# Optimization experiments

Measured on AMD Instinct MI355X. Metric: run time of the kernel, lower is better.

Reference implementation:

```python
import jax, jax.numpy as jnp
import numpy as np

B, F, U, G = 2048, 512, 512, 64
REG_STRENGTH = 1.0


def setup_inputs() -> dict:
    key = jax.random.key(0)
    k0, k1, k2, k3, k4 = jax.random.split(key, 5)
    x = jax.random.normal(k0, (B, F), dtype=jnp.float32)
    gid = jax.random.randint(k1, (B,), 0, G, dtype=jnp.int64)
    # glorot-normal-ish scale for kernels: sqrt(2/(fan_in+fan_out))
    glorot = np.sqrt(2.0 / (U + F)).astype(np.float32)
    w_mu = jax.random.normal(k2, (G, U, F), dtype=jnp.float32) * glorot
    b_mu = jax.random.normal(k3, (G, U), dtype=jnp.float32) * 0.05  # 'random_normal' init
    w0_mu = jax.random.normal(k4, (U, F), dtype=jnp.float32) * glorot
    b0_mu = jnp.zeros((U,), dtype=jnp.float32)
    return {"x": x, "gid": gid, "w_mu": w_mu, "b_mu": b_mu, "w0_mu": w0_mu, "b0_mu": b0_mu}


def reference(x, gid, w_mu, b_mu, w0_mu, b0_mu):
    # Hard top-1 routing: per-sample weight matrix gather, [B, U, F]
    w = jnp.take(w_mu, gid, axis=0)
    b = jnp.take(b_mu, gid, axis=0)  # [B, U]
    # Batched matvec: 'Bup,Bp->Bu'
    outputs = jnp.einsum("buf,bf->bu", w, x) + b  # use_bias=True, activation=None
    # L2 prior regularization loss (added via add_loss in the original)
    w_loss = jnp.sum(jnp.square(w - w0_mu[None]))  # sum over axes [1,2] then batch
    b_loss = jnp.sum(jnp.square(b - b0_mu[None]))
    reg_loss = REG_STRENGTH * (w_loss + b_loss)
    return outputs, reg_loss
```

## Files before the change

kernel.cpp:

```cpp
#include <hip/hip_runtime.h>
#include <hip/hip_bf16.h>

#define B_SZ 2048
#define F_SZ 512
#define U_SZ 512
#define G_SZ 64
#define REG_STRENGTH 1.0f

#define BM 32
#define BN 64
#define BK 32
#define ZSPLIT 2
#define NTILES (U_SZ / BN)
#define THREADS 128


__global__ __launch_bounds__(1024) void prep_kernel(
    const int* __restrict__ gid, float* __restrict__ wsf,
    int* __restrict__ counts, int* __restrict__ rowstart,
    int* __restrict__ order) {
  __shared__ int cnt_s[G_SZ];
  __shared__ int cur_s[G_SZ];
  const int tid = threadIdx.x;

  if (tid < G_SZ) cnt_s[tid] = 0;
  if (tid == 0) wsf[0] = 0.0f;
  __syncthreads();

  for (int b = tid; b < B_SZ; b += 1024) atomicAdd(&cnt_s[gid[b]], 1);
  __syncthreads();

  if (tid == 0) {
    int run = 0;
    for (int g = 0; g < G_SZ; ++g) { cur_s[g] = run; run += cnt_s[g]; }
  }
  __syncthreads();

  if (tid < G_SZ) { counts[tid] = cnt_s[tid]; rowstart[tid] = cur_s[tid]; }
  __syncthreads();

  for (int b = tid; b < B_SZ; b += 1024) {
    int pos = atomicAdd(&cur_s[gid[b]], 1);
    order[pos] = b;
  }
}

__global__ __launch_bounds__(THREADS) void gemm_kernel(
    const float* __restrict__ x, const float* __restrict__ w_mu,
    const float* __restrict__ b_mu, const float* __restrict__ w0_mu,
    const float* __restrict__ b0_mu, float* __restrict__ out,
    float* __restrict__ wsf, const int* __restrict__ counts,
    const int* __restrict__ rowstart, const int* __restrict__ order) {
  const int g = blockIdx.y;
  const int cnt = counts[g];
  if (cnt == 0) return;
  const int z = blockIdx.z;
  const int n0 = blockIdx.x * BN;
  const int rs = rowstart[g];
  const int tid = threadIdx.x;

  const int tn = tid & 15;
  const int tmc = tid >> 4;
  const int sr = tid >> 3;
  const int skq = tid & 7;
  const int kb = skq * 4;

  __shared__ __align__(16) float Xs[BK][BM + 4];
  __shared__ __align__(16) float Ws[BK][BN + 4];

  const float* __restrict__ Wg = w_mu + (size_t)g * (U_SZ * F_SZ);
  const bool do_reg = (z == 0);
  float regp = 0.0f;

  if (do_reg && blockIdx.x == 0) {
    const float4 bm4 = *(const float4*)(b_mu + (g << 9) + tid * 4);
    const float4 b04 = *(const float4*)(b0_mu + tid * 4);
    float dx = bm4.x - b04.x, dy = bm4.y - b04.y;
    float dz = bm4.z - b04.z, dw = bm4.w - b04.w;
    regp += dx * dx + dy * dy + dz * dz + dw * dw;
  }

  bool first_pass = true;
  for (int r0 = z * BM; r0 < cnt; r0 += BM * ZSPLIT) {
    float acc[4][4] = {};
    int rA = r0 + sr;      if (rA >= cnt) rA = cnt - 1;
    int rB = r0 + sr + 16; if (rB >= cnt) rB = cnt - 1;
    const float* __restrict__ xrowA = x + (size_t)order[rs + rA] * F_SZ;
    const float* __restrict__ xrowB = x + (size_t)order[rs + rB] * F_SZ;

    float4 xpA = *(const float4*)(xrowA + kb);
    float4 xpB = *(const float4*)(xrowB + kb);
    float4 wp[4];
#pragma unroll
    for (int m = 0; m < 4; ++m)
      wp[m] = *(const float4*)(Wg + (size_t)(n0 + sr + 16 * m) * F_SZ + kb);

    for (int kc = 0; kc < F_SZ; kc += BK) {
      __syncthreads();
      Xs[kb + 0][sr] = xpA.x; Xs[kb + 1][sr] = xpA.y;
      Xs[kb + 2][sr] = xpA.z; Xs[kb + 3][sr] = xpA.w;
      Xs[kb + 0][sr + 16] = xpB.x; Xs[kb + 1][sr + 16] = xpB.y;
      Xs[kb + 2][sr + 16] = xpB.z; Xs[kb + 3][sr + 16] = xpB.w;
#pragma unroll
      for (int m = 0; m < 4; ++m) {
        const int u = sr + 16 * m;
        Ws[kb + 0][u] = wp[m].x; Ws[kb + 1][u] = wp[m].y;
        Ws[kb + 2][u] = wp[m].z; Ws[kb + 3][u] = wp[m].w;
      }
      if (do_reg && first_pass) {
#pragma unroll
        for (int m = 0; m < 4; ++m) {
          const float4 w04 = *(const float4*)(
              w0_mu + (size_t)(n0 + sr + 16 * m) * F_SZ + kc + kb);
          float dx = wp[m].x - w04.x, dy = wp[m].y - w04.y;
          float dz = wp[m].z - w04.z, dw = wp[m].w - w04.w;
          regp += dx * dx + dy * dy + dz * dz + dw * dw;
        }
      }
      __syncthreads();
      if (kc + BK < F_SZ) {
        const int ko = kc + BK + kb;
        xpA = *(const float4*)(xrowA + ko);
        xpB = *(const float4*)(xrowB + ko);
#pragma unroll
        for (int m = 0; m < 4; ++m)
          wp[m] = *(const float4*)(Wg + (size_t)(n0 + sr + 16 * m) * F_SZ + ko);
      }
#pragma unroll
      for (int kk = 0; kk < BK; ++kk) {
        const float4 av = *(const float4*)&Xs[kk][tmc * 4];
        const float4 bv = *(const float4*)&Ws[kk][tn * 4];
        const float a[4] = {av.x, av.y, av.z, av.w};
        const float b[4] = {bv.x, bv.y, bv.z, bv.w};
#pragma unroll
        for (int i = 0; i < 4; ++i)
#pragma unroll
          for (int j = 0; j < 4; ++j) acc[i][j] += a[i] * b[j];
      }
    }

    const float4 bias = *(const float4*)(b_mu + (g << 9) + n0 + tn * 4);
#pragma unroll
    for (int i = 0; i < 4; ++i) {
      const int r = r0 + tmc * 4 + i;
      if (r < cnt) {
        float4 o;
        o.x = acc[i][0] + bias.x;
        o.y = acc[i][1] + bias.y;
        o.z = acc[i][2] + bias.z;
        o.w = acc[i][3] + bias.w;
        *(float4*)(out + (size_t)order[rs + r] * U_SZ + n0 + tn * 4) = o;
      }
    }
    first_pass = false;
  }

  if (do_reg) {
    __syncthreads();
    float* red = &Xs[0][0];
    red[tid] = regp;
    __syncthreads();
    for (int s = 64; s > 0; s >>= 1) {
      if (tid < s) red[tid] += red[tid + s];
      __syncthreads();
    }
    if (tid == 0) atomicAdd(wsf, (float)cnt * red[0]);
  }
}

__global__ void finalize_kernel(const float* __restrict__ wsf,
                                float* __restrict__ out) {
  out[(size_t)B_SZ * U_SZ] = REG_STRENGTH * wsf[0];
}

extern "C" void kernel_launch(void* const* d_in, const int* in_sizes, int n_in,
                              void* d_out, int out_size, void* d_ws, size_t ws_size,
                              hipStream_t stream) {
  const float* x     = (const float*)d_in[0];
  const int*   gid   = (const int*)d_in[1];
  const float* w_mu  = (const float*)d_in[2];
  const float* b_mu  = (const float*)d_in[3];
  const float* w0_mu = (const float*)d_in[4];
  const float* b0_mu = (const float*)d_in[5];
  float* out = (float*)d_out;

  float* wsf      = (float*)d_ws;
  int*   counts   = (int*)d_ws + 2;
  int*   rowstart = (int*)d_ws + 2 + G_SZ;
  int*   order    = (int*)d_ws + 2 + 2 * G_SZ;

  prep_kernel<<<1, 1024, 0, stream>>>(gid, wsf, counts, rowstart, order);
  gemm_kernel<<<dim3(NTILES, G_SZ, ZSPLIT), THREADS, 0, stream>>>(
      x, w_mu, b_mu, w0_mu, b0_mu, out, wsf, counts, rowstart, order);
  finalize_kernel<<<1, 1, 0, stream>>>(wsf, out);
}
```

Before: 142.0 us.

## Use bf16 MFMA with chunk-scheduled grid and fused last-block finalize

Replaces the fp32 FMA tiled GEMM with bf16 MFMA 16x16x32 instructions. Inputs are converted to bf16 when staged into shared memory. The grid is rebuilt from a per-group chunk list of 64 rows, built in prep, instead of a fixed group-by-zsplit grid. The finalize kernel is dropped in favour of a last-block ticket, which saves one launch and cuts idle blocks. The cost is bf16 precision loss in the outputs, which may break tolerance, plus extra register use.

After: 174.8 us. 1.23x slower.

```diff
diff --git a/kernel.cpp b/kernel.cpp
--- a/kernel.cpp
+++ b/kernel.cpp
@@ -7,170 +7,210 @@
 #define G_SZ 64
 #define REG_STRENGTH 1.0f
 
-#define BM 32
+#define BM 64
 #define BN 64
-#define BK 32
-#define ZSPLIT 2
+#define BK 64
 #define NTILES (U_SZ / BN)
-#define THREADS 128
-
+#define MAXCHUNKS (B_SZ / BM + G_SZ)
+#define XSTR 72
+#define WSTR 72
+
+typedef __attribute__((ext_vector_type(8))) short bf16x8;
+typedef __attribute__((ext_vector_type(4))) float f32x4;
+
+#define WS_WSF      0
+#define WS_TICKET   1
+#define WS_NCH      2
+#define WS_COUNTS   4
+#define WS_ROWSTART (4 + G_SZ)
+#define WS_ORDER    (4 + 2 * G_SZ)
+#define WS_CHUNKS   (4 + 2 * G_SZ + B_SZ)
+
+__device__ __forceinline__ unsigned short f2bf(float f) {
+  unsigned u = __float_as_uint(f);
+  u += 0x7FFFu + ((u >> 16) & 1u);
+  return (unsigned short)(u >> 16);
+}
 
 __global__ __launch_bounds__(1024) void prep_kernel(
-    const int* __restrict__ gid, float* __restrict__ wsf,
-    int* __restrict__ counts, int* __restrict__ rowstart,
-    int* __restrict__ order) {
+    const int* __restrict__ gid, int* __restrict__ wsi) {
   __shared__ int cnt_s[G_SZ];
   __shared__ int cur_s[G_SZ];
+  __shared__ int chk_s[G_SZ];
   const int tid = threadIdx.x;
 
   if (tid < G_SZ) cnt_s[tid] = 0;
-  if (tid == 0) wsf[0] = 0.0f;
+  if (tid == 0) { ((float*)wsi)[WS_WSF] = 0.0f; wsi[WS_TICKET] = 0; }
   __syncthreads();
 
   for (int b = tid; b < B_SZ; b += 1024) atomicAdd(&cnt_s[gid[b]], 1);
   __syncthreads();
 
   if (tid == 0) {
-    int run = 0;
-    for (int g = 0; g < G_SZ; ++g) { cur_s[g] = run; run += cnt_s[g]; }
-  }
-  __syncthreads();
-
-  if (tid < G_SZ) { counts[tid] = cnt_s[tid]; rowstart[tid] = cur_s[tid]; }
+    int run = 0, crun = 0;
+    for (int g = 0; g < G_SZ; ++g) {
+      cur_s[g] = run;
+      chk_s[g] = crun;
+      run += cnt_s[g];
+      crun += (cnt_s[g] + BM - 1) / BM;
+    }
+    wsi[WS_NCH] = crun;
+  }
+  __syncthreads();
+
+  if (tid < G_SZ) {
+    wsi[WS_COUNTS + tid] = cnt_s[tid];
+    wsi[WS_ROWSTART + tid] = cur_s[tid];
+    const int nch = (cnt_s[tid] + BM - 1) / BM;
+    const int cs = chk_s[tid];
+    for (int i = 0; i < nch; ++i)
+      wsi[WS_CHUNKS + cs + i] = tid | ((i * BM) << 8);
+  }
   __syncthreads();
 
   for (int b = tid; b < B_SZ; b += 1024) {
     int pos = atomicAdd(&cur_s[gid[b]], 1);
-    order[pos] = b;
-  }
-}
-
-__global__ __launch_bounds__(THREADS) void gemm_kernel(
+    wsi[WS_ORDER + pos] = b;
+  }
+}
+
+__global__ __launch_bounds__(256) void gemm_kernel(
     const float* __restrict__ x, const float* __restrict__ w_mu,
     const float* __restrict__ b_mu, const float* __restrict__ w0_mu,
     const float* __restrict__ b0_mu, float* __restrict__ out,
-    float* __restrict__ wsf, const int* __restrict__ counts,
-    const int* __restrict__ rowstart, const int* __restrict__ order) {
-  const int g = blockIdx.y;
-  const int cnt = counts[g];
-  if (cnt == 0) return;
-  const int z = blockIdx.z;
-  const int n0 = blockIdx.x * BN;
-  const int rs = rowstart[g];
+    int* __restrict__ wsi) {
   const int tid = threadIdx.x;
-
-  const int tn = tid & 15;
-  const int tmc = tid >> 4;
-  const int sr = tid >> 3;
-  const int skq = tid & 7;
-  const int kb = skq * 4;
-
-  __shared__ __align__(16) float Xs[BK][BM + 4];
-  __shared__ __align__(16) float Ws[BK][BN + 4];
-
-  const float* __restrict__ Wg = w_mu + (size_t)g * (U_SZ * F_SZ);
-  const bool do_reg = (z == 0);
-  float regp = 0.0f;
-
-  if (do_reg && blockIdx.x == 0) {
-    const float4 bm4 = *(const float4*)(b_mu + (g << 9) + tid * 4);
-    const float4 b04 = *(const float4*)(b0_mu + tid * 4);
-    float dx = bm4.x - b04.x, dy = bm4.y - b04.y;
-    float dz = bm4.z - b04.z, dw = bm4.w - b04.w;
-    regp += dx * dx + dy * dy + dz * dz + dw * dw;
-  }
-
-  bool first_pass = true;
-  for (int r0 = z * BM; r0 < cnt; r0 += BM * ZSPLIT) {
-    float acc[4][4] = {};
-    int rA = r0 + sr;      if (rA >= cnt) rA = cnt - 1;
-    int rB = r0 + sr + 16; if (rB >= cnt) rB = cnt - 1;
-    const float* __restrict__ xrowA = x + (size_t)order[rs + rA] * F_SZ;
-    const float* __restrict__ xrowB = x + (size_t)order[rs + rB] * F_SZ;
-
-    float4 xpA = *(const float4*)(xrowA + kb);
-    float4 xpB = *(const float4*)(xrowB + kb);
-    float4 wp[4];
-#pragma unroll
-    for (int m = 0; m < 4; ++m)
-      wp[m] = *(const float4*)(Wg + (size_t)(n0 + sr + 16 * m) * F_SZ + kb);
+  const int lane = tid & 63;
+  const int wave = tid >> 6;
+  const int nch = wsi[WS_NCH];
+  const int slot = blockIdx.y;
+
+  __shared__ __align__(16) unsigned short Xbf[BM][XSTR];
+  __shared__ __align__(16) unsigned short Wbf[BN][WSTR];
+  __shared__ float redw[4];
+
+  if (slot < nch) {
+    const int entry = wsi[WS_CHUNKS + slot];
+    const int g = entry & 0xFF;
+    const int r0 = entry >> 8;
+    const int cnt = wsi[WS_COUNTS + g];
+    const int rs = wsi[WS_ROWSTART + g];
+    const int n0 = blockIdx.x * BN;
+    const bool do_reg = (r0 == 0);
+    const float* __restrict__ Wg = w_mu + (size_t)g * (U_SZ * F_SZ);
+    float regp = 0.0f;
+
+    if (do_reg && blockIdx.x == 0) {
+      for (int i = tid; i < U_SZ; i += 256) {
+        float d = b_mu[(g << 9) + i] - b0_mu[i];
+        regp += d * d;
+      }
+    }
+
+    const int sr = tid >> 4;
+    const int skq = tid & 15;
+    const float* xptr[4];
+    const float* wptr[4];
+#pragma unroll
+    for (int j = 0; j < 4; ++j) {
+      int r = r0 + sr + 16 * j;
+      if (r >= cnt) r = cnt - 1;
+      xptr[j] = x + (size_t)wsi[WS_ORDER + rs + r] * F_SZ + skq * 4;
+      wptr[j] = Wg + (size_t)(n0 + sr + 16 * j) * F_SZ + skq * 4;
+    }
+
+    const int fl = lane & 15;
+    const int fq = lane >> 4;
+    const unsigned short* aF = &Xbf[wave * 16 + fl][fq * 8];
+    const unsigned short* bF = &Wbf[fl][fq * 8];
+
+    f32x4 acc[4] = {{0.f, 0.f, 0.f, 0.f}, {0.f, 0.f, 0.f, 0.f},
+                    {0.f, 0.f, 0.f, 0.f}, {0.f, 0.f, 0.f, 0.f}};
+
+    float4 xp[4], wp[4], w0p[4];
+#pragma unroll
+    for (int j = 0; j < 4; ++j) {
+      xp[j] = *(const float4*)(xptr[j]);
+      wp[j] = *(const float4*)(wptr[j]);
+    }
+    if (do_reg)
+#pragma unroll
+      for (int j = 0; j < 4; ++j)
+        w0p[j] = *(const float4*)(w0_mu + (size_t)(n0 + sr + 16 * j) * F_SZ + skq * 4);
 
     for (int kc = 0; kc < F_SZ; kc += BK) {
       __syncthreads();
-      Xs[kb + 0][sr] = xpA.x; Xs[kb + 1][sr] = xpA.y;
-      Xs[kb + 2][sr] = xpA.z; Xs[kb + 3][sr] = xpA.w;
-      Xs[kb + 0][sr + 16] = xpB.x; Xs[kb + 1][sr + 16] = xpB.y;
-      Xs[kb + 2][sr + 16] = xpB.z; Xs[kb + 3][sr + 16] = xpB.w;
-#pragma unroll
-      for (int m = 0; m < 4; ++m) {
-        const int u = sr + 16 * m;
-        Ws[kb + 0][u] = wp[m].x; Ws[kb + 1][u] = wp[m].y;
-        Ws[kb + 2][u] = wp[m].z; Ws[kb + 3][u] = wp[m].w;
-      }
-      if (do_reg && first_pass) {
-#pragma unroll
-        for (int m = 0; m < 4; ++m) {
-          const float4 w04 = *(const float4*)(
-              w0_mu + (size_t)(n0 + sr + 16 * m) * F_SZ + kc + kb);
-          float dx = wp[m].x - w04.x, dy = wp[m].y - w04.y;
-          float dz = wp[m].z - w04.z, dw = wp[m].w - w04.w;
+#pragma unroll
+      for (int j = 0; j < 4; ++j) {
+        const int row = sr + 16 * j;
+        *(ushort4*)&Xbf[row][skq * 4] =
+            make_ushort4(f2bf(xp[j].x), f2bf(xp[j].y), f2bf(xp[j].z), f2bf(xp[j].w));
+        *(ushort4*)&Wbf[row][skq * 4] =
+            make_ushort4(f2bf(wp[j].x), f2bf(wp[j].y), f2bf(wp[j].z), f2bf(wp[j].w));
+        if (do_reg) {
+          float dx = wp[j].x - w0p[j].x, dy = wp[j].y - w0p[j].y;
+          float dz = wp[j].z - w0p[j].z, dw = wp[j].w - w0p[j].w;
           regp += dx * dx + dy * dy + dz * dz + dw * dw;
         }
       }
       __syncthreads();
       if (kc + BK < F_SZ) {
-        const int ko = kc + BK + kb;
-        xpA = *(const float4*)(xrowA + ko);
-        xpB = *(const float4*)(xrowB + ko);
-#pragma unroll
-        for (int m = 0; m < 4; ++m)
-          wp[m] = *(const float4*)(Wg + (size_t)(n0 + sr + 16 * m) * F_SZ + ko);
-      }
-#pragma unroll
-      for (int kk = 0; kk < BK; ++kk) {
-        const float4 av = *(const float4*)&Xs[kk][tmc * 4];
-        const float4 bv = *(const float4*)&Ws[kk][tn * 4];
-        const float a[4] = {av.x, av.y, av.z, av.w};
-        const float b[4] = {bv.x, bv.y, bv.z, bv.w};
-#pragma unroll
-        for (int i = 0; i < 4; ++i)
-#pragma unroll
-          for (int j = 0; j < 4; ++j) acc[i][j] += a[i] * b[j];
-      }
-    }
-
-    const float4 bias = *(const float4*)(b_mu + (g << 9) + n0 + tn * 4);
+        const int ko = kc + BK;
+#pragma unroll
+        for (int j = 0; j < 4; ++j) {
+          xp[j] = *(const float4*)(xptr[j] + ko);
+          wp[j] = *(const float4*)(wptr[j] + ko);
+        }
+        if (do_reg)
+#pragma unroll
+          for (int j = 0; j < 4; ++j)
+            w0p[j] = *(const float4*)(w0_mu + (size_t)(n0 + sr + 16 * j) * F_SZ + ko + skq * 4);
+      }
+#pragma unroll
+      for (int ks = 0; ks < 2; ++ks) {
+        const bf16x8 a = *(const bf16x8*)(aF + ks * 32);
+#pragma unroll
+        for (int t = 0; t < 4; ++t) {
+          const bf16x8 b = *(const bf16x8*)(bF + t * 16 * WSTR + ks * 32);
+          acc[t] = __builtin_amdgcn_mfma_f32_16x16x32_bf16(a, b, acc[t], 0, 0, 0);
+        }
+      }
+    }
+
+    int orow[4];
 #pragma unroll
     for (int i = 0; i < 4; ++i) {
-      const int r = r0 + tmc * 4 + i;
-      if (r < cnt) {
-        float4 o;
-        o.x = acc[i][0] + bias.x;
-        o.y = acc[i][1] + bias.y;
-        o.z = acc[i][2] + bias.z;
-        o.w = acc[i][3] + bias.w;
-        *(float4*)(out + (size_t)order[rs + r] * U_SZ + n0 + tn * 4) = o;
-      }
-    }
-    first_pass = false;
-  }
-
-  if (do_reg) {
-    __syncthreads();
-    float* red = &Xs[0][0];
-    red[tid] = regp;
-    __syncthreads();
-    for (int s = 64; s > 0; s >>= 1) {
-      if (tid < s) red[tid] += red[tid + s];
+      const int r = r0 + wave * 16 + fq * 4 + i;
+      orow[i] = (r < cnt) ? wsi[WS_ORDER + rs + r] : -1;
+    }
+#pragma unroll
+    for (int t = 0; t < 4; ++t) {
+      const int gcol = n0 + 16 * t + fl;
+      const float bias = b_mu[(g << 9) + gcol];
+#pragma unroll
+      for (int i = 0; i < 4; ++i)
+        if (orow[i] >= 0) out[(size_t)orow[i] * U_SZ + gcol] = acc[t][i] + bias;
+    }
+
+    if (do_reg) {
+#pragma unroll
+      for (int off = 32; off > 0; off >>= 1) regp += __shfl_down(regp, off);
+      if (lane == 0) redw[wave] = regp;
       __syncthreads();
-    }
-    if (tid == 0) atomicAdd(wsf, (float)cnt * red[0]);
-  }
-}
-
-__global__ void finalize_kernel(const float* __restrict__ wsf,
-                                float* __restrict__ out) {
-  out[(size_t)B_SZ * U_SZ] = REG_STRENGTH * wsf[0];
+      if (tid == 0)
+        atomicAdd((float*)&wsi[WS_WSF],
+                  (float)cnt * (redw[0] + redw[1] + redw[2] + redw[3]));
+    }
+  }
+
+  __threadfence();
+  if (tid == 0) {
+    const int total_blocks = gridDim.x * gridDim.y;
+    if (atomicAdd(&wsi[WS_TICKET], 1) == total_blocks - 1) {
+      float v = atomicAdd((float*)&wsi[WS_WSF], 0.0f);
+      out[(size_t)B_SZ * U_SZ] = REG_STRENGTH * v;
+    }
+  }
 }
 
 extern "C" void kernel_launch(void* const* d_in, const int* in_sizes, int n_in,
@@ -183,14 +223,9 @@
   const float* w0_mu = (const float*)d_in[4];
   const float* b0_mu = (const float*)d_in[5];
   float* out = (float*)d_out;
-
-  float* wsf      = (float*)d_ws;
-  int*   counts   = (int*)d_ws + 2;
-  int*   rowstart = (int*)d_ws + 2 + G_SZ;
-  int*   order    = (int*)d_ws + 2 + 2 * G_SZ;
-
-  prep_kernel<<<1, 1024, 0, stream>>>(gid, wsf, counts, rowstart, order);
-  gemm_kernel<<<dim3(NTILES, G_SZ, ZSPLIT), THREADS, 0, stream>>>(
-      x, w_mu, b_mu, w0_mu, b0_mu, out, wsf, counts, rowstart, order);
-  finalize_kernel<<<1, 1, 0, stream>>>(wsf, out);
-}
+  int* wsi = (int*)d_ws;
+
+  prep_kernel<<<1, 1024, 0, stream>>>(gid, wsi);
+  gemm_kernel<<<dim3(NTILES, MAXCHUNKS), 256, 0, stream>>>(
+      x, w_mu, b_mu, w0_mu, b0_mu, out, wsi);
+}
```
